# Kernel optimization log

Hardware: AMD Instinct MI355X
Metric: run time of the kernel (lower is better)

Reference implementation:

```python
import jax, jax.numpy as jnp
from jax import lax
import numpy as np

SCORE_THRESH = 0.05
NMS_THRESH = 0.5
MAX_DET = 100
MIN_SIZE = 0.01
BBOX_CLIP = float(np.log(1000.0 / 16.0))
NEG = -1e10


def setup_inputs() -> dict:
    key = jax.random.key(0)
    ks = jax.random.split(key, 12)
    N, IN, REP, C = 2000, 256 * 7 * 7, 1024, 91
    box_features = jax.random.normal(ks[0], (N, IN), jnp.float32)
    x1 = jax.random.uniform(ks[1], (N,), jnp.float32, 0.0, 1000.0)
    y1 = jax.random.uniform(ks[2], (N,), jnp.float32, 0.0, 600.0)
    bw = jax.random.uniform(ks[3], (N,), jnp.float32, 16.0, 200.0)
    bh = jax.random.uniform(ks[4], (N,), jnp.float32, 16.0, 180.0)
    proposals = jnp.stack([x1, y1, x1 + bw, y1 + bh], axis=1)
    W1 = jax.random.normal(ks[5], (IN, REP), jnp.float32) * 0.01
    b1 = jnp.zeros((REP,), jnp.float32)
    W2 = jax.random.normal(ks[6], (REP, REP), jnp.float32) * 0.03
    b2 = jnp.zeros((REP,), jnp.float32)
    Wc = jax.random.normal(ks[7], (REP, C), jnp.float32) * 0.1
    bc = jax.random.normal(ks[8], (C,), jnp.float32) * 0.5
    Wr = jax.random.normal(ks[9], (REP, 4 * C), jnp.float32) * 0.01
    br = jnp.zeros((4 * C,), jnp.float32)
    return dict(box_features=box_features, proposals=proposals,
                W1=W1, b1=b1, W2=W2, b2=b2, Wc=Wc, bc=bc, Wr=Wr, br=br,
                image_h=800, image_w=1216)


def _nms(boxes, scores):
    """Greedy NMS with fixed trip count; scores already masked to NEG for invalid."""
    M = boxes.shape[0]
    areas = (boxes[:, 2] - boxes[:, 0]) * (boxes[:, 3] - boxes[:, 1])
    idxs = jnp.arange(M)

    def step(sm, _):
        i = jnp.argmax(sm)
        valid = sm[i] > NEG * 0.5
        b = boxes[i]
        xx1 = jnp.maximum(b[0], boxes[:, 0]); yy1 = jnp.maximum(b[1], boxes[:, 1])
        xx2 = jnp.minimum(b[2], boxes[:, 2]); yy2 = jnp.minimum(b[3], boxes[:, 3])
        inter = jnp.clip(xx2 - xx1, 0.0) * jnp.clip(yy2 - yy1, 0.0)
        iou = inter / (areas[i] + areas - inter + 1e-9)
        suppress = (iou > NMS_THRESH) | (idxs == i)
        sm = jnp.where(valid, jnp.where(suppress, NEG, sm), sm)
        return sm, jnp.where(valid, i, -1)

    _, keep = lax.scan(step, scores, None, length=MAX_DET)
    return keep  # [MAX_DET] int, -1 for padding


def reference(box_features, proposals, W1, b1, W2, b2, Wc, bc, Wr, br, image_h, image_w):
    N = box_features.shape[0]
    C = Wc.shape[1]
    # box head MLP (Linear+ReLU x2) and predictors
    h = jax.nn.relu(box_features @ W1 + b1)
    h = jax.nn.relu(h @ W2 + b2)
    class_logits = h @ Wc + bc                      # [N, C]
    box_reg = (h @ Wr + br).reshape(N, C, 4)        # [N, C, 4]
    # box decode (weights 10,10,5,5) against proposals
    pw = proposals[:, 2] - proposals[:, 0]
    ph = proposals[:, 3] - proposals[:, 1]
    pcx = proposals[:, 0] + 0.5 * pw
    pcy = proposals[:, 1] + 0.5 * ph
    dx = box_reg[..., 0] / 10.0
    dy = box_reg[..., 1] / 10.0
    dw = jnp.minimum(box_reg[..., 2] / 5.0, BBOX_CLIP)
    dh = jnp.minimum(box_reg[..., 3] / 5.0, BBOX_CLIP)
    cx = dx * pw[:, None] + pcx[:, None]
    cy = dy * ph[:, None] + pcy[:, None]
    w = jnp.exp(dw) * pw[:, None]
    hh = jnp.exp(dh) * ph[:, None]
    boxes = jnp.stack([cx - 0.5 * w, cy - 0.5 * hh, cx + 0.5 * w, cy + 0.5 * hh], axis=-1)
    scores = jax.nn.softmax(class_logits, axis=-1)
    # clip to image
    Wim = jnp.float32(image_w); Him = jnp.float32(image_h)
    boxes = jnp.stack([jnp.clip(boxes[..., 0], 0.0, Wim),
                       jnp.clip(boxes[..., 1], 0.0, Him),
                       jnp.clip(boxes[..., 2], 0.0, Wim),
                       jnp.clip(boxes[..., 3], 0.0, Him)], axis=-1)
    # drop background class, flatten to [N*(C-1)]
    boxes = boxes[:, 1:].reshape(-1, 4)
    scores = scores[:, 1:].reshape(-1)
    labels = jnp.broadcast_to(jnp.arange(1, C, dtype=jnp.int32), (N, C - 1)).reshape(-1)
    # score threshold + remove small boxes (as masking, static shapes)
    bw = boxes[:, 2] - boxes[:, 0]
    bh = boxes[:, 3] - boxes[:, 1]
    valid = (scores > SCORE_THRESH) & (bw >= MIN_SIZE) & (bh >= MIN_SIZE)
    sm = jnp.where(valid, scores, NEG)
    # class-aware (batched) NMS via per-class coordinate offsets
    off = labels.astype(boxes.dtype) * (jnp.maximum(Wim, Him) + 1.0)
    keep = _nms(boxes + off[:, None], sm)
    mask = keep >= 0
    idx = jnp.maximum(keep, 0)
    out_boxes = jnp.take(boxes, idx, axis=0) * mask[:, None]
    out_scores = jnp.take(scores, idx) * mask
    out_labels = jnp.take(labels, idx) * mask.astype(jnp.int32)
    return out_boxes, out_scores, out_labels
```

## Files before the change

kernel.cpp:

```cpp
#include <hip/hip_runtime.h>

#define TM 128
#define TN 128
#define TKK 16
#define CPC 2000
#define SPC 100
#define NCLS 90

typedef __attribute__((ext_vector_type(8))) short bf16x8;
typedef __attribute__((ext_vector_type(4))) float f32x4;

__device__ __forceinline__ unsigned short f2bf_rne(float f) {
    unsigned u = __float_as_uint(f);
    return (unsigned short)((u + 0x7FFFu + ((u >> 16) & 1u)) >> 16);
}
__device__ __forceinline__ unsigned short f2bf_trunc(float f) {
    return (unsigned short)(__float_as_uint(f) >> 16);
}
__device__ __forceinline__ float bfhi_f32(float f) {
    return __uint_as_float(__float_as_uint(f) & 0xFFFF0000u);
}
__device__ __forceinline__ void async_load16(const void* g, void* l) {
    __builtin_amdgcn_global_load_lds((const __attribute__((address_space(1))) unsigned int*)g,
                                     (__attribute__((address_space(3))) unsigned int*)l, 16, 0, 0);
}

__global__ __launch_bounds__(256) void split_transpose(
    const float* __restrict__ W, unsigned short* __restrict__ Thi,
    unsigned short* __restrict__ Tlo, int K, int N)
{
    __shared__ float tile[32][33];
    const int kt = blockIdx.x * 32, nt = blockIdx.y * 32;
    const int tx = threadIdx.x & 31, ty = threadIdx.x >> 5;
#pragma unroll
    for (int j = 0; j < 4; ++j) {
        int k = kt + ty + j * 8, n = nt + tx;
        tile[ty + j * 8][tx] = (k < K && n < N) ? W[(size_t)k * N + n] : 0.f;
    }
    __syncthreads();
#pragma unroll
    for (int j = 0; j < 4; ++j) {
        int n = nt + ty + j * 8, k = kt + tx;
        if (n < N && k < K) {
            float f = tile[tx][ty + j * 8];
            Thi[(size_t)n * K + k] = f2bf_trunc(f);
            Tlo[(size_t)n * K + k] = f2bf_rne(f - bfhi_f32(f));
        }
    }
}

__global__ __launch_bounds__(256) void split_transpose2(
    const float* __restrict__ Wa, const float* __restrict__ Wb, int Na, int Nb,
    unsigned short* __restrict__ Thi, unsigned short* __restrict__ Tlo, int K)
{
    const int N = Na + Nb;
    __shared__ float tile[32][33];
    const int kt = blockIdx.x * 32, nt = blockIdx.y * 32;
    const int tx = threadIdx.x & 31, ty = threadIdx.x >> 5;
#pragma unroll
    for (int j = 0; j < 4; ++j) {
        int k = kt + ty + j * 8, n = nt + tx;
        float v = 0.f;
        if (k < K && n < N)
            v = (n < Na) ? Wa[(size_t)k * Na + n] : Wb[(size_t)k * Nb + (n - Na)];
        tile[ty + j * 8][tx] = v;
    }
    __syncthreads();
#pragma unroll
    for (int j = 0; j < 4; ++j) {
        int n = nt + ty + j * 8, k = kt + tx;
        if (n < N && k < K) {
            float f = tile[tx][ty + j * 8];
            Thi[(size_t)n * K + k] = f2bf_trunc(f);
            Tlo[(size_t)n * K + k] = f2bf_rne(f - bfhi_f32(f));
        }
    }
}

__global__ __launch_bounds__(256) void gemm_bf16x3(
    const float* __restrict__ A, const unsigned short* __restrict__ Bhi,
    const unsigned short* __restrict__ Blo, float* __restrict__ C,
    int M, int N, int K, int klen)
{
    __shared__ unsigned short Ah[4096], Al[4096], Bh[4096], Bl[4096];
    const int tid = threadIdx.x;
    const int wv = tid >> 6, ln = tid & 63;
    const int q = ln >> 4, lm = ln & 15;
    const int m0 = blockIdx.y * 128, n0 = blockIdx.x * 128;
    const int k0 = blockIdx.z * klen, k1 = k0 + klen;
    const int arow_t = (wv >> 1) * 64, bcol_t = (wv & 1) * 64;

    f32x4 acc[4][4];
#pragma unroll
    for (int i = 0; i < 4; ++i)
#pragma unroll
        for (int j = 0; j < 4; ++j) acc[i][j] = (f32x4)0.f;

    const int r = tid >> 1, h = tid & 1;
    const bool arow_ok = (m0 + r) < M;
    const float* Arow = A + (size_t)(m0 + r) * K + h * 16;

    for (int kt = k0; kt < k1; kt += 32) {
#pragma unroll
        for (int i = 0; i < 2; ++i) {
            int c = i * 256 + wv * 64 + ln;
            int kq = c >> 7;
            int gn = n0 + (c & 127); if (gn >= N) gn = N - 1;
            async_load16(Bhi + (size_t)gn * K + kt + kq * 8, &Bh[(size_t)(i * 256 + wv * 64) * 8]);
            async_load16(Blo + (size_t)gn * K + kt + kq * 8, &Bl[(size_t)(i * 256 + wv * 64) * 8]);
        }
        float f[16];
        if (arow_ok) {
            const float4* ap = reinterpret_cast<const float4*>(Arow + kt);
#pragma unroll
            for (int e = 0; e < 4; ++e) {
                float4 v = ap[e];
                f[e * 4 + 0] = v.x; f[e * 4 + 1] = v.y; f[e * 4 + 2] = v.z; f[e * 4 + 3] = v.w;
            }
        } else {
#pragma unroll
            for (int e = 0; e < 16; ++e) f[e] = 0.f;
        }
        bf16x8 h0, h1, l0, l1;
#pragma unroll
        for (int e = 0; e < 8; ++e) {
            h0[e] = (short)f2bf_trunc(f[e]);
            h1[e] = (short)f2bf_trunc(f[e + 8]);
            l0[e] = (short)f2bf_rne(f[e] - bfhi_f32(f[e]));
            l1[e] = (short)f2bf_rne(f[e + 8] - bfhi_f32(f[e + 8]));
        }
        *(bf16x8*)&Ah[(size_t)((h * 2 + 0) * 128 + r) * 8] = h0;
        *(bf16x8*)&Ah[(size_t)((h * 2 + 1) * 128 + r) * 8] = h1;
        *(bf16x8*)&Al[(size_t)((h * 2 + 0) * 128 + r) * 8] = l0;
        *(bf16x8*)&Al[(size_t)((h * 2 + 1) * 128 + r) * 8] = l1;
        __syncthreads();

        bf16x8 afh[4], afl[4], bfh[4], bfl[4];
#pragma unroll
        for (int mi = 0; mi < 4; ++mi) {
            int c = q * 128 + arow_t + mi * 16 + lm;
            afh[mi] = *(const bf16x8*)&Ah[(size_t)c * 8];
            afl[mi] = *(const bf16x8*)&Al[(size_t)c * 8];
        }
#pragma unroll
        for (int ni = 0; ni < 4; ++ni) {
            int c = q * 128 + bcol_t + ni * 16 + lm;
            bfh[ni] = *(const bf16x8*)&Bh[(size_t)c * 8];
            bfl[ni] = *(const bf16x8*)&Bl[(size_t)c * 8];
        }
#pragma unroll
        for (int mi = 0; mi < 4; ++mi)
#pragma unroll
            for (int ni = 0; ni < 4; ++ni) {
                acc[mi][ni] = __builtin_amdgcn_mfma_f32_16x16x32_bf16(afh[mi], bfh[ni], acc[mi][ni], 0, 0, 0);
                acc[mi][ni] = __builtin_amdgcn_mfma_f32_16x16x32_bf16(afl[mi], bfh[ni], acc[mi][ni], 0, 0, 0);
                acc[mi][ni] = __builtin_amdgcn_mfma_f32_16x16x32_bf16(afh[mi], bfl[ni], acc[mi][ni], 0, 0, 0);
            }
        __syncthreads();
    }

    float* Cz = C + (size_t)blockIdx.z * (size_t)M * (size_t)N;
#pragma unroll
    for (int mi = 0; mi < 4; ++mi)
#pragma unroll
        for (int ni = 0; ni < 4; ++ni)
#pragma unroll
            for (int ri = 0; ri < 4; ++ri) {
                int rr = m0 + arow_t + mi * 16 + q * 4 + ri;
                int cc = n0 + bcol_t + ni * 16 + lm;
                if (rr < M && cc < N) Cz[(size_t)rr * N + cc] = acc[mi][ni][ri];
            }
}

__global__ __launch_bounds__(256) void gemm_f32(
    const float* __restrict__ A, const float* __restrict__ B,
    const float* __restrict__ bias, float* __restrict__ C,
    int M, int N, int K, int ksplit, int relu)
{
    __shared__ float As[TKK][TM + 4];
    __shared__ float Bs[TKK][TN + 4];
    const int tid = threadIdx.x;
    const int tx = tid & 15, ty = tid >> 4;
    const int m0 = blockIdx.y * TM, n0 = blockIdx.x * TN;
    const int z = blockIdx.z;
    const int kstart = z * ksplit;
    const int kend = (kstart + ksplit < K) ? (kstart + ksplit) : K;
    float* Cz = C + (size_t)z * (size_t)M * (size_t)N;
    const bool nvec = ((N & 3) == 0);

    float acc[8][8];
#pragma unroll
    for (int i = 0; i < 8; ++i)
#pragma unroll
        for (int j = 0; j < 8; ++j) acc[i][j] = 0.f;

    for (int kt = kstart; kt < kend; kt += TKK) {
#pragma unroll
        for (int l = 0; l < 2; ++l) {
            int idx = tid + l * 256;
            int rr = idx >> 2, kq = idx & 3;
            float4 v = make_float4(0.f, 0.f, 0.f, 0.f);
            int gr = m0 + rr;
            if (gr < M)
                v = *reinterpret_cast<const float4*>(A + (size_t)gr * K + kt + (kq << 2));
            As[(kq << 2) + 0][rr] = v.x;
            As[(kq << 2) + 1][rr] = v.y;
            As[(kq << 2) + 2][rr] = v.z;
            As[(kq << 2) + 3][rr] = v.w;
        }
#pragma unroll
        for (int l = 0; l < 2; ++l) {
            int idx = tid + l * 256;
            int kk = idx >> 5, nq = idx & 31;
            int gn = n0 + (nq << 2);
            const float* bp = B + (size_t)(kt + kk) * N + gn;
            float4 v;
            if (nvec && gn + 3 < N) {
                v = *reinterpret_cast<const float4*>(bp);
            } else {
                v.x = (gn + 0 < N) ? bp[0] : 0.f;
                v.y = (gn + 1 < N) ? bp[1] : 0.f;
                v.z = (gn + 2 < N) ? bp[2] : 0.f;
                v.w = (gn + 3 < N) ? bp[3] : 0.f;
            }
            *reinterpret_cast<float4*>(&Bs[kk][nq << 2]) = v;
        }
        __syncthreads();
#pragma unroll
        for (int kk = 0; kk < TKK; ++kk) {
            float a[8], b[8];
            *reinterpret_cast<float4*>(&a[0]) = *reinterpret_cast<const float4*>(&As[kk][ty * 8]);
            *reinterpret_cast<float4*>(&a[4]) = *reinterpret_cast<const float4*>(&As[kk][ty * 8 + 4]);
            *reinterpret_cast<float4*>(&b[0]) = *reinterpret_cast<const float4*>(&Bs[kk][tx * 4]);
            *reinterpret_cast<float4*>(&b[4]) = *reinterpret_cast<const float4*>(&Bs[kk][64 + tx * 4]);
#pragma unroll
            for (int i = 0; i < 8; ++i)
#pragma unroll
                for (int j = 0; j < 8; ++j)
                    acc[i][j] = fmaf(a[i], b[j], acc[i][j]);
        }
        __syncthreads();
    }
#pragma unroll
    for (int i = 0; i < 8; ++i) {
        int gr = m0 + ty * 8 + i;
        if (gr >= M) continue;
#pragma unroll
        for (int j = 0; j < 8; ++j) {
            int gc = n0 + ((j < 4) ? (tx * 4 + j) : (64 + tx * 4 + (j - 4)));
            if (gc >= N) continue;
            float v = acc[i][j];
            if (bias) v += bias[gc];
            if (relu) v = fmaxf(v, 0.f);
            Cz[(size_t)gr * N + gc] = v;
        }
    }
}

__global__ void combine_bias_act(const float* __restrict__ P, const float* __restrict__ bias,
                                 float* __restrict__ H, int total, int N, int nsplit,
                                 int pstride, int relu)
{
    int i = blockIdx.x * blockDim.x + threadIdx.x;
    if (i >= total) return;
    float s = P[i];
    for (int j = 1; j < nsplit; ++j) s += P[i + (size_t)j * (size_t)pstride];
    s += bias[i % N];
    if (relu) s = fmaxf(s, 0.f);
    H[i] = s;
}

__global__ void combine_head(const float* __restrict__ P, const float* __restrict__ bc,
                             const float* __restrict__ br, float* __restrict__ H,
                             int total, int nsplit, int pstride)
{
    int i = blockIdx.x * blockDim.x + threadIdx.x;
    if (i >= total) return;
    float s = P[i];
    for (int j = 1; j < nsplit; ++j) s += P[i + (size_t)j * (size_t)pstride];
    int col = i % 455;
    s += (col < 91) ? bc[col] : br[col - 91];
    H[i] = s;
}

__device__ __forceinline__ float scalar_dim(const int* p)
{
    int iv = *p;
    return (iv > 0 && iv < (1 << 20)) ? (float)iv : *reinterpret_cast<const float*>(p);
}

__global__ __launch_bounds__(128) void decode_compact(
    const float* __restrict__ logits, int lstr, const float* __restrict__ breg, int bstr,
    const float4* __restrict__ proposals, const int* __restrict__ ihp,
    const int* __restrict__ iwp,
    float4* __restrict__ cbox, float* __restrict__ cscore, int* __restrict__ cn,
    int* __restrict__ ccnt)
{
    const int n = blockIdx.x;
    const int c = threadIdx.x;
    __shared__ float sl[91];
    __shared__ float s_max, s_sum;
    if (c < 91) sl[c] = logits[(size_t)n * lstr + c];
    __syncthreads();
    if (c == 0) {
        float m = sl[0];
        for (int i = 1; i < 91; ++i) m = fmaxf(m, sl[i]);
        float s = 0.f;
        for (int i = 0; i < 91; ++i) s += expf(sl[i] - m);
        s_max = m; s_sum = s;
    }
    __syncthreads();
    if (c < 1 || c >= 91) return;

    const float score = expf(sl[c] - s_max) / s_sum;
    const float Wim = scalar_dim(iwp), Him = scalar_dim(ihp);
    float4 p = proposals[n];
    float pw = p.z - p.x, ph = p.w - p.y;
    float pcx = p.x + 0.5f * pw, pcy = p.y + 0.5f * ph;
    const float* r4 = breg + (size_t)n * bstr + c * 4;
    float dxv = r4[0] / 10.f, dyv = r4[1] / 10.f;
    const float BCLIP = 4.135166556742356f;
    float dwv = fminf(r4[2] / 5.f, BCLIP);
    float dhv = fminf(r4[3] / 5.f, BCLIP);
    float cx = dxv * pw + pcx, cy = dyv * ph + pcy;
    float w = expf(dwv) * pw, hh = expf(dhv) * ph;
    float x1 = cx - 0.5f * w, y1 = cy - 0.5f * hh;
    float x2 = cx + 0.5f * w, y2 = cy + 0.5f * hh;
    x1 = fminf(fmaxf(x1, 0.f), Wim);
    y1 = fminf(fmaxf(y1, 0.f), Him);
    x2 = fminf(fmaxf(x2, 0.f), Wim);
    y2 = fminf(fmaxf(y2, 0.f), Him);
    float bw = x2 - x1, bh = y2 - y1;
    if (score > 0.05f && bw >= 0.01f && bh >= 0.01f) {
        int cls = c - 1;
        int pos = atomicAdd(&ccnt[cls], 1);
        if (pos < CPC) {
            cbox[cls * CPC + pos] = make_float4(x1, y1, x2, y2);
            cscore[cls * CPC + pos] = score;
            cn[cls * CPC + pos] = n;
        }
    }
}

__global__ __launch_bounds__(256) void nms_class(
    const float4* __restrict__ cbox, const float* __restrict__ cscore,
    const int* __restrict__ cn, const int* __restrict__ ccnt,
    float4* __restrict__ sbox, float* __restrict__ sscore,
    unsigned long long* __restrict__ skey, int* __restrict__ scnt)
{
    const int cls = blockIdx.x;
    const int tid = threadIdx.x;
    int cnt = ccnt[cls]; if (cnt > CPC) cnt = CPC;

    __shared__ float4 cb[CPC];
    __shared__ unsigned long long keys[CPC];
    __shared__ unsigned long long red[4];
    __shared__ float4 selsh;
    __shared__ int selidx_sh;

    for (int i = tid; i < cnt; i += 256) {
        cb[i] = cbox[cls * CPC + i];
        unsigned int sb = __float_as_uint(cscore[cls * CPC + i]);
        sb ^= (sb >> 31) ? 0xFFFFFFFFu : 0x80000000u;
        unsigned int flat = (unsigned)cn[cls * CPC + i] * 90u + (unsigned)cls;
        keys[i] = ((unsigned long long)sb << 32) | (unsigned long long)(0xFFFFFFFFu - flat);
    }
    __syncthreads();

    int sel = 0;
    while (sel < SPC) {
        unsigned long long best = 0ull;
        for (int i = tid; i < cnt; i += 256) {
            unsigned long long k = keys[i];
            if (k > best) best = k;
        }
#pragma unroll
        for (int d = 32; d >= 1; d >>= 1) {
            unsigned long long o = __shfl_down(best, d, 64);
            if (o > best) best = o;
        }
        if ((tid & 63) == 0) red[tid >> 6] = best;
        __syncthreads();
        unsigned long long gbest = red[0];
        if (red[1] > gbest) gbest = red[1];
        if (red[2] > gbest) gbest = red[2];
        if (red[3] > gbest) gbest = red[3];
        if (gbest == 0ull) break;
        for (int i = tid; i < cnt; i += 256)
            if (keys[i] == gbest) { selsh = cb[i]; selidx_sh = i; }
        __syncthreads();
        float4 s = selsh;
        const int si = selidx_sh;
        const float sa = (s.z - s.x) * (s.w - s.y);
        if (tid == 0) {
            sbox[cls * SPC + sel] = s;
            unsigned int sb = (unsigned int)(gbest >> 32);
            sb ^= (sb >> 31) ? 0x80000000u : 0xFFFFFFFFu;
            sscore[cls * SPC + sel] = __uint_as_float(sb);
            skey[cls * SPC + sel] = gbest;
        }
        for (int i = tid; i < cnt; i += 256) {
            float4 b = cb[i];
            float xx1 = fmaxf(s.x, b.x), yy1 = fmaxf(s.y, b.y);
            float xx2 = fminf(s.z, b.z), yy2 = fminf(s.w, b.w);
            float inter = fmaxf(xx2 - xx1, 0.f) * fmaxf(yy2 - yy1, 0.f);
            float area = (b.z - b.x) * (b.w - b.y);
            if (3.f * inter > sa + area + 1e-9f || i == si) keys[i] = 0ull;
        }
        ++sel;
        __syncthreads();
    }
    if (tid == 0) scnt[cls] = sel;
}

__global__ __launch_bounds__(128) void nms_merge(
    const float4* __restrict__ sbox, const float* __restrict__ sscore,
    const unsigned long long* __restrict__ skey, const int* __restrict__ scnt,
    float* __restrict__ out)
{
    const int tid = threadIdx.x;
    __shared__ int head[NCLS];
    __shared__ unsigned long long red[2];
    __shared__ int selc_sh;
    if (tid < NCLS) head[tid] = 0;
    __syncthreads();

    for (int k = 0; k < 100; ++k) {
        unsigned long long key = 0ull;
        if (tid < NCLS && head[tid] < scnt[tid]) key = skey[tid * SPC + head[tid]];
        unsigned long long mykey = key;
#pragma unroll
        for (int d = 32; d >= 1; d >>= 1) {
            unsigned long long o = __shfl_down(key, d, 64);
            if (o > key) key = o;
        }
        if ((tid & 63) == 0) red[tid >> 6] = key;
        if (tid == 0) selc_sh = -1;
        __syncthreads();
        unsigned long long gbest = red[0] > red[1] ? red[0] : red[1];
        if (gbest != 0ull && mykey == gbest) selc_sh = tid;
        __syncthreads();
        const int c = selc_sh;
        if (tid == 0) {
            if (c >= 0) {
                int h = head[c];
                float4 b = sbox[c * SPC + h];
                out[k * 4 + 0] = b.x; out[k * 4 + 1] = b.y;
                out[k * 4 + 2] = b.z; out[k * 4 + 3] = b.w;
                out[400 + k] = sscore[c * SPC + h];
                out[500 + k] = (float)(c + 1);
            } else {
                out[k * 4 + 0] = 0.f; out[k * 4 + 1] = 0.f;
                out[k * 4 + 2] = 0.f; out[k * 4 + 3] = 0.f;
                out[400 + k] = 0.f; out[500 + k] = 0.f;
            }
        }
        if (c >= 0 && tid == c) head[c]++;
        __syncthreads();
    }
}

extern "C" void kernel_launch(void* const* d_in, const int* in_sizes, int n_in,
                              void* d_out, int out_size, void* d_ws, size_t ws_size,
                              hipStream_t stream)
{
    const float* bf    = (const float*)d_in[0];
    const float* props = (const float*)d_in[1];
    const float* W1    = (const float*)d_in[2];
    const float* b1    = (const float*)d_in[3];
    const float* W2    = (const float*)d_in[4];
    const float* b2    = (const float*)d_in[5];
    const float* Wc    = (const float*)d_in[6];
    const float* bc    = (const float*)d_in[7];
    const float* Wr    = (const float*)d_in[8];
    const float* br    = (const float*)d_in[9];
    const int*   ihp   = (const int*)d_in[10];
    const int*   iwp   = (const int*)d_in[11];
    float* ws  = (float*)d_ws;
    float* out = (float*)d_out;

    const size_t MN   = 2000ull * 1024ull;
    const size_t NLOG = 2000ull * 91ull;
    const size_t NREG = 2000ull * 364ull;
    const size_t NHEAD = 2000ull * 455ull;
    const size_t ws_floats = ws_size / 4;

    const size_t BT1F = 1024ull * 12544ull / 2;
    const size_t WT2F = 1024ull * 1024ull / 2;
    const size_t WHF  = 455ull * 1024ull / 2;
    const size_t NMSF = (size_t)NCLS * CPC * 6 + (size_t)NCLS * SPC * 7 + 256;
    const size_t PF   = 4 * MN;
    const size_t NEED = 2 * BT1F + 2 * WT2F + 2 * WHF + 2 * MN + NHEAD + NMSF + PF + 64;

    if (ws_floats >= NEED) {
        unsigned short* BT1hi = (unsigned short*)ws;
        unsigned short* BT1lo = (unsigned short*)(ws + BT1F);
        unsigned short* WT2hi = (unsigned short*)(ws + 2 * BT1F);
        unsigned short* WT2lo = (unsigned short*)(ws + 2 * BT1F + WT2F);
        unsigned short* WHhi  = (unsigned short*)(ws + 2 * BT1F + 2 * WT2F);
        unsigned short* WHlo  = (unsigned short*)(ws + 2 * BT1F + 2 * WT2F + WHF);
        float* H1   = ws + 2 * BT1F + 2 * WT2F + 2 * WHF;
        float* H2   = H1 + MN;
        float* HEAD = H2 + MN;
        float* CBOX   = HEAD + NHEAD;
        float* CSCORE = CBOX + (size_t)NCLS * CPC * 4;
        int*   CN     = (int*)(CSCORE + (size_t)NCLS * CPC);
        float* SBOX   = (float*)(CN + (size_t)NCLS * CPC);
        float* SSCORE = SBOX + (size_t)NCLS * SPC * 4;
        unsigned long long* SKEY = (unsigned long long*)(SSCORE + (size_t)NCLS * SPC);
        int*   CCNT = (int*)(SKEY + (size_t)NCLS * SPC);
        int*   SCNT = CCNT + NCLS;
        float* P = (float*)(SCNT + NCLS + 62);

        split_transpose<<<dim3(392, 32), 256, 0, stream>>>(W1, BT1hi, BT1lo, 12544, 1024);
        split_transpose<<<dim3(32, 32), 256, 0, stream>>>(W2, WT2hi, WT2lo, 1024, 1024);
        split_transpose2<<<dim3(32, 15), 256, 0, stream>>>(Wc, Wr, 91, 364, WHhi, WHlo, 1024);
        gemm_bf16x3<<<dim3(8, 16, 4), 256, 0, stream>>>(bf, BT1hi, BT1lo, P,
                                                        2000, 1024, 12544, 3136);
        combine_bias_act<<<(int)((MN + 255) / 256), 256, 0, stream>>>(P, b1, H1,
                                                        (int)MN, 1024, 4, (int)MN, 1);
        gemm_bf16x3<<<dim3(8, 16, 4), 256, 0, stream>>>(H1, WT2hi, WT2lo, P,
                                                        2000, 1024, 1024, 256);
        combine_bias_act<<<(int)((MN + 255) / 256), 256, 0, stream>>>(P, b2, H2,
                                                        (int)MN, 1024, 4, (int)MN, 1);
        gemm_bf16x3<<<dim3(4, 16, 8), 256, 0, stream>>>(H2, WHhi, WHlo, P,
                                                        2000, 455, 1024, 128);
        combine_head<<<(int)((NHEAD + 255) / 256), 256, 0, stream>>>(P, bc, br, HEAD,
                                                        (int)NHEAD, 8, (int)NHEAD);
        hipMemsetAsync(CCNT, 0, 2 * NCLS * sizeof(int), stream);
        decode_compact<<<2000, 128, 0, stream>>>(HEAD, 455, HEAD + 91, 455,
                                                 (const float4*)props, ihp, iwp,
                                                 (float4*)CBOX, CSCORE, CN, CCNT);
        nms_class<<<NCLS, 256, 0, stream>>>((const float4*)CBOX, CSCORE, CN, CCNT,
                                            (float4*)SBOX, SSCORE, SKEY, SCNT);
        nms_merge<<<1, 128, 0, stream>>>((const float4*)SBOX, SSCORE, SKEY, SCNT, out);
        return;
    }

    const size_t NMSF2 = (size_t)NCLS * CPC * 6 + (size_t)NCLS * SPC * 7 + 256;
    const size_t TAILF = 2 * MN + NLOG + NREG + NMSF2;
    int z1 = 2;
    if (ws_floats >= TAILF + 8 * MN) z1 = 8;
    else if (ws_floats >= TAILF + 4 * MN) z1 = 4;
    const size_t REUSE = (size_t)z1 * MN;
    int zh = (REUSE >= 8 * NREG) ? 8 : 4;

    float* P      = ws;
    float* H1     = P + REUSE;
    float* H2     = H1 + MN;
    float* LOG    = H2 + MN;
    float* BREG   = LOG + NLOG;
    float* CBOX   = BREG + NREG;
    float* CSCORE = CBOX + (size_t)NCLS * CPC * 4;
    int*   CN     = (int*)(CSCORE + (size_t)NCLS * CPC);
    float* SBOX   = (float*)(CN + (size_t)NCLS * CPC);
    float* SSCORE = SBOX + (size_t)NCLS * SPC * 4;
    unsigned long long* SKEY = (unsigned long long*)(SSCORE + (size_t)NCLS * SPC);
    int*   CCNT   = (int*)(SKEY + (size_t)NCLS * SPC);
    int*   SCNT   = CCNT + NCLS;

    gemm_f32<<<dim3(8, 16, z1), 256, 0, stream>>>(bf, W1, nullptr, P,
                                                  2000, 1024, 12544, 12544 / z1, 0);
    combine_bias_act<<<(int)((MN + 255) / 256), 256, 0, stream>>>(P, b1, H1,
                                                  (int)MN, 1024, z1, (int)MN, 1);
    gemm_f32<<<dim3(8, 16, 4), 256, 0, stream>>>(H1, W2, nullptr, P,
                                                 2000, 1024, 1024, 256, 0);
    combine_bias_act<<<(int)((MN + 255) / 256), 256, 0, stream>>>(P, b2, H2,
                                                 (int)MN, 1024, 4, (int)MN, 1);
    gemm_f32<<<dim3(1, 16, zh), 256, 0, stream>>>(H2, Wc, nullptr, P,
                                                  2000, 91, 1024, 1024 / zh, 0);
    combine_bias_act<<<(int)((NLOG + 255) / 256), 256, 0, stream>>>(P, bc, LOG,
                                                  (int)NLOG, 91, zh, (int)NLOG, 0);
    gemm_f32<<<dim3(3, 16, zh), 256, 0, stream>>>(H2, Wr, nullptr, P,
                                                  2000, 364, 1024, 1024 / zh, 0);
    combine_bias_act<<<(int)((NREG + 255) / 256), 256, 0, stream>>>(P, br, BREG,
                                                  (int)NREG, 364, zh, (int)NREG, 0);
    hipMemsetAsync(CCNT, 0, 2 * NCLS * sizeof(int), stream);
    decode_compact<<<2000, 128, 0, stream>>>(LOG, 91, BREG, 364,
                                             (const float4*)props, ihp, iwp,
                                             (float4*)CBOX, CSCORE, CN, CCNT);
    nms_class<<<NCLS, 256, 0, stream>>>((const float4*)CBOX, CSCORE, CN, CCNT,
                                        (float4*)SBOX, SSCORE, SKEY, SCNT);
    nms_merge<<<1, 128, 0, stream>>>((const float4*)SBOX, SSCORE, SKEY, SCNT, out);
}
```

Baseline: 761.6 us.

## Shrink GEMM tiles to 64x128, swizzle LDS, pre-split activations into bf16 hi/lo

The bf16x3 GEMMs now use 64x128 block tiles (each wave computes 64x32), doubling the block count and setting occupancy hints with launch_bounds(256,4). LDS layouts use an XOR swizzle to reduce bank conflicts. For the second and third GEMMs, the combine kernel writes the activations already split into bf16 hi/lo, so the GEMM loads A asynchronously into LDS and skips the per-tile conversion. The trade-off is more global reloads of B from the smaller M tiles and more, smaller blocks.

Result: no change. 751.0 us (-1.4%).

```diff
diff --git a/kernel.cpp b/kernel.cpp
--- a/kernel.cpp
+++ b/kernel.cpp
@@ -1,11 +1,11 @@
 #include <hip/hip_runtime.h>
 
+#define CPC 2000
+#define SPC 100
+#define NCLS 90
 #define TM 128
 #define TN 128
 #define TKK 16
-#define CPC 2000
-#define SPC 100
-#define NCLS 90
 
 typedef __attribute__((ext_vector_type(8))) short bf16x8;
 typedef __attribute__((ext_vector_type(4))) float f32x4;
@@ -24,6 +24,7 @@
     __builtin_amdgcn_global_load_lds((const __attribute__((address_space(1))) unsigned int*)g,
                                      (__attribute__((address_space(3))) unsigned int*)l, 16, 0, 0);
 }
+__device__ __forceinline__ int swz(int c) { return c ^ ((c >> 3) & 3); }
 
 __global__ __launch_bounds__(256) void split_transpose(
     const float* __restrict__ W, unsigned short* __restrict__ Thi,
@@ -77,81 +78,75 @@
     }
 }
 
-__global__ __launch_bounds__(256) void gemm_bf16x3(
+__global__ __launch_bounds__(256, 4) void gemm_bf16x3_f32a(
     const float* __restrict__ A, const unsigned short* __restrict__ Bhi,
     const unsigned short* __restrict__ Blo, float* __restrict__ C,
     int M, int N, int K, int klen)
 {
-    __shared__ unsigned short Ah[4096], Al[4096], Bh[4096], Bl[4096];
+    __shared__ unsigned short Ah[2048], Al[2048], Bh[4096], Bl[4096];
     const int tid = threadIdx.x;
     const int wv = tid >> 6, ln = tid & 63;
     const int q = ln >> 4, lm = ln & 15;
-    const int m0 = blockIdx.y * 128, n0 = blockIdx.x * 128;
+    const int m0 = blockIdx.y * 64, n0 = blockIdx.x * 128;
     const int k0 = blockIdx.z * klen, k1 = k0 + klen;
-    const int arow_t = (wv >> 1) * 64, bcol_t = (wv & 1) * 64;
-
-    f32x4 acc[4][4];
+    const int bcol_t = wv * 32;
+
+    f32x4 acc[4][2];
 #pragma unroll
     for (int i = 0; i < 4; ++i)
 #pragma unroll
-        for (int j = 0; j < 4; ++j) acc[i][j] = (f32x4)0.f;
-
-    const int r = tid >> 1, h = tid & 1;
-    const bool arow_ok = (m0 + r) < M;
-    const float* Arow = A + (size_t)(m0 + r) * K + h * 16;
+        for (int j = 0; j < 2; ++j) acc[i][j] = (f32x4)0.f;
+
+    const int r = tid >> 2, h = tid & 3;
+    int gr = m0 + r; if (gr >= M) gr = M - 1;
+    const float* Arow = A + (size_t)gr * K + h * 8;
+    const int apc = swz(tid);
+
+    unsigned bsrc[2];
+#pragma unroll
+    for (int i = 0; i < 2; ++i) {
+        int s = i * 256 + tid;
+        int gn = n0 + (s >> 2); if (gn >= N) gn = N - 1;
+        int qe = (s & 3) ^ ((s >> 3) & 3);
+        bsrc[i] = (unsigned)gn * (unsigned)K + (unsigned)(qe * 8);
+    }
 
     for (int kt = k0; kt < k1; kt += 32) {
 #pragma unroll
         for (int i = 0; i < 2; ++i) {
-            int c = i * 256 + wv * 64 + ln;
-            int kq = c >> 7;
-            int gn = n0 + (c & 127); if (gn >= N) gn = N - 1;
-            async_load16(Bhi + (size_t)gn * K + kt + kq * 8, &Bh[(size_t)(i * 256 + wv * 64) * 8]);
-            async_load16(Blo + (size_t)gn * K + kt + kq * 8, &Bl[(size_t)(i * 256 + wv * 64) * 8]);
-        }
-        float f[16];
-        if (arow_ok) {
-            const float4* ap = reinterpret_cast<const float4*>(Arow + kt);
-#pragma unroll
-            for (int e = 0; e < 4; ++e) {
-                float4 v = ap[e];
-                f[e * 4 + 0] = v.x; f[e * 4 + 1] = v.y; f[e * 4 + 2] = v.z; f[e * 4 + 3] = v.w;
-            }
-        } else {
-#pragma unroll
-            for (int e = 0; e < 16; ++e) f[e] = 0.f;
-        }
-        bf16x8 h0, h1, l0, l1;
+            async_load16(Bhi + bsrc[i] + kt, &Bh[(i * 256 + wv * 64) * 8]);
+            async_load16(Blo + bsrc[i] + kt, &Bl[(i * 256 + wv * 64) * 8]);
+        }
+        float4 v0 = *reinterpret_cast<const float4*>(Arow + kt);
+        float4 v1 = *reinterpret_cast<const float4*>(Arow + kt + 4);
+        float f[8] = {v0.x, v0.y, v0.z, v0.w, v1.x, v1.y, v1.z, v1.w};
+        bf16x8 hi, lo;
 #pragma unroll
         for (int e = 0; e < 8; ++e) {
-            h0[e] = (short)f2bf_trunc(f[e]);
-            h1[e] = (short)f2bf_trunc(f[e + 8]);
-            l0[e] = (short)f2bf_rne(f[e] - bfhi_f32(f[e]));
-            l1[e] = (short)f2bf_rne(f[e + 8] - bfhi_f32(f[e + 8]));
-        }
-        *(bf16x8*)&Ah[(size_t)((h * 2 + 0) * 128 + r) * 8] = h0;
-        *(bf16x8*)&Ah[(size_t)((h * 2 + 1) * 128 + r) * 8] = h1;
-        *(bf16x8*)&Al[(size_t)((h * 2 + 0) * 128 + r) * 8] = l0;
-        *(bf16x8*)&Al[(size_t)((h * 2 + 1) * 128 + r) * 8] = l1;
-        __syncthreads();
-
-        bf16x8 afh[4], afl[4], bfh[4], bfl[4];
+            hi[e] = (short)f2bf_trunc(f[e]);
+            lo[e] = (short)f2bf_rne(f[e] - bfhi_f32(f[e]));
+        }
+        *(bf16x8*)&Ah[apc * 8] = hi;
+        *(bf16x8*)&Al[apc * 8] = lo;
+        __syncthreads();
+
+        bf16x8 afh[4], afl[4], bfh[2], bfl[2];
 #pragma unroll
         for (int mi = 0; mi < 4; ++mi) {
-            int c = q * 128 + arow_t + mi * 16 + lm;
-            afh[mi] = *(const bf16x8*)&Ah[(size_t)c * 8];
-            afl[mi] = *(const bf16x8*)&Al[(size_t)c * 8];
-        }
-#pragma unroll
-        for (int ni = 0; ni < 4; ++ni) {
-            int c = q * 128 + bcol_t + ni * 16 + lm;
-            bfh[ni] = *(const bf16x8*)&Bh[(size_t)c * 8];
-            bfl[ni] = *(const bf16x8*)&Bl[(size_t)c * 8];
+            int p = swz((mi * 16 + lm) * 4 + q);
+            afh[mi] = *(const bf16x8*)&Ah[p * 8];
+            afl[mi] = *(const bf16x8*)&Al[p * 8];
+        }
+#pragma unroll
+        for (int ni = 0; ni < 2; ++ni) {
+            int p = swz((bcol_t + ni * 16 + lm) * 4 + q);
+            bfh[ni] = *(const bf16x8*)&Bh[p * 8];
+            bfl[ni] = *(const bf16x8*)&Bl[p * 8];
         }
 #pragma unroll
         for (int mi = 0; mi < 4; ++mi)
 #pragma unroll
-            for (int ni = 0; ni < 4; ++ni) {
+            for (int ni = 0; ni < 2; ++ni) {
                 acc[mi][ni] = __builtin_amdgcn_mfma_f32_16x16x32_bf16(afh[mi], bfh[ni], acc[mi][ni], 0, 0, 0);
                 acc[mi][ni] = __builtin_amdgcn_mfma_f32_16x16x32_bf16(afl[mi], bfh[ni], acc[mi][ni], 0, 0, 0);
                 acc[mi][ni] = __builtin_amdgcn_mfma_f32_16x16x32_bf16(afh[mi], bfl[ni], acc[mi][ni], 0, 0, 0);
@@ -163,10 +158,91 @@
 #pragma unroll
     for (int mi = 0; mi < 4; ++mi)
 #pragma unroll
-        for (int ni = 0; ni < 4; ++ni)
+        for (int ni = 0; ni < 2; ++ni)
 #pragma unroll
             for (int ri = 0; ri < 4; ++ri) {
-                int rr = m0 + arow_t + mi * 16 + q * 4 + ri;
+                int rr = m0 + mi * 16 + q * 4 + ri;
+                int cc = n0 + bcol_t + ni * 16 + lm;
+                if (rr < M && cc < N) Cz[(size_t)rr * N + cc] = acc[mi][ni][ri];
+            }
+}
+
+__global__ __launch_bounds__(256, 4) void gemm_bf16x3_sa(
+    const unsigned short* __restrict__ Ahi_g, const unsigned short* __restrict__ Alo_g,
+    const unsigned short* __restrict__ Bhi, const unsigned short* __restrict__ Blo,
+    float* __restrict__ C, int M, int N, int K, int klen)
+{
+    __shared__ unsigned short Ah[2048], Al[2048], Bh[4096], Bl[4096];
+    const int tid = threadIdx.x;
+    const int wv = tid >> 6, ln = tid & 63;
+    const int q = ln >> 4, lm = ln & 15;
+    const int m0 = blockIdx.y * 64, n0 = blockIdx.x * 128;
+    const int k0 = blockIdx.z * klen, k1 = k0 + klen;
+    const int bcol_t = wv * 32;
+
+    f32x4 acc[4][2];
+#pragma unroll
+    for (int i = 0; i < 4; ++i)
+#pragma unroll
+        for (int j = 0; j < 2; ++j) acc[i][j] = (f32x4)0.f;
+
+    {
+    }
+    int agr = m0 + (tid >> 2); if (agr >= M) agr = M - 1;
+    const int aqe = (tid & 3) ^ ((tid >> 3) & 3);
+    const unsigned asrc = (unsigned)agr * (unsigned)K + (unsigned)(aqe * 8);
+
+    unsigned bsrc[2];
+#pragma unroll
+    for (int i = 0; i < 2; ++i) {
+        int s = i * 256 + tid;
+        int gn = n0 + (s >> 2); if (gn >= N) gn = N - 1;
+        int qe = (s & 3) ^ ((s >> 3) & 3);
+        bsrc[i] = (unsigned)gn * (unsigned)K + (unsigned)(qe * 8);
+    }
+
+    for (int kt = k0; kt < k1; kt += 32) {
+        async_load16(Ahi_g + asrc + kt, &Ah[(wv * 64) * 8]);
+        async_load16(Alo_g + asrc + kt, &Al[(wv * 64) * 8]);
+#pragma unroll
+        for (int i = 0; i < 2; ++i) {
+            async_load16(Bhi + bsrc[i] + kt, &Bh[(i * 256 + wv * 64) * 8]);
+            async_load16(Blo + bsrc[i] + kt, &Bl[(i * 256 + wv * 64) * 8]);
+        }
+        __syncthreads();
+
+        bf16x8 afh[4], afl[4], bfh[2], bfl[2];
+#pragma unroll
+        for (int mi = 0; mi < 4; ++mi) {
+            int p = swz((mi * 16 + lm) * 4 + q);
+            afh[mi] = *(const bf16x8*)&Ah[p * 8];
+            afl[mi] = *(const bf16x8*)&Al[p * 8];
+        }
+#pragma unroll
+        for (int ni = 0; ni < 2; ++ni) {
+            int p = swz((bcol_t + ni * 16 + lm) * 4 + q);
+            bfh[ni] = *(const bf16x8*)&Bh[p * 8];
+            bfl[ni] = *(const bf16x8*)&Bl[p * 8];
+        }
+#pragma unroll
+        for (int mi = 0; mi < 4; ++mi)
+#pragma unroll
+            for (int ni = 0; ni < 2; ++ni) {
+                acc[mi][ni] = __builtin_amdgcn_mfma_f32_16x16x32_bf16(afh[mi], bfh[ni], acc[mi][ni], 0, 0, 0);
+                acc[mi][ni] = __builtin_amdgcn_mfma_f32_16x16x32_bf16(afl[mi], bfh[ni], acc[mi][ni], 0, 0, 0);
+                acc[mi][ni] = __builtin_amdgcn_mfma_f32_16x16x32_bf16(afh[mi], bfl[ni], acc[mi][ni], 0, 0, 0);
+            }
+        __syncthreads();
+    }
+
+    float* Cz = C + (size_t)blockIdx.z * (size_t)M * (size_t)N;
+#pragma unroll
+    for (int mi = 0; mi < 4; ++mi)
+#pragma unroll
+        for (int ni = 0; ni < 2; ++ni)
+#pragma unroll
+            for (int ri = 0; ri < 4; ++ri) {
+                int rr = m0 + mi * 16 + q * 4 + ri;
                 int cc = n0 + bcol_t + ni * 16 + lm;
                 if (rr < M && cc < N) Cz[(size_t)rr * N + cc] = acc[mi][ni][ri];
             }
@@ -200,9 +276,9 @@
             int idx = tid + l * 256;
             int rr = idx >> 2, kq = idx & 3;
             float4 v = make_float4(0.f, 0.f, 0.f, 0.f);
-            int gr = m0 + rr;
-            if (gr < M)
-                v = *reinterpret_cast<const float4*>(A + (size_t)gr * K + kt + (kq << 2));
+            int grr = m0 + rr;
+            if (grr < M)
+                v = *reinterpret_cast<const float4*>(A + (size_t)grr * K + kt + (kq << 2));
             As[(kq << 2) + 0][rr] = v.x;
             As[(kq << 2) + 1][rr] = v.y;
             As[(kq << 2) + 2][rr] = v.z;
@@ -243,8 +319,8 @@
     }
 #pragma unroll
     for (int i = 0; i < 8; ++i) {
-        int gr = m0 + ty * 8 + i;
-        if (gr >= M) continue;
+        int grr = m0 + ty * 8 + i;
+        if (grr >= M) continue;
 #pragma unroll
         for (int j = 0; j < 8; ++j) {
             int gc = n0 + ((j < 4) ? (tx * 4 + j) : (64 + tx * 4 + (j - 4)));
@@ -252,7 +328,7 @@
             float v = acc[i][j];
             if (bias) v += bias[gc];
             if (relu) v = fmaxf(v, 0.f);
-            Cz[(size_t)gr * N + gc] = v;
+            Cz[(size_t)grr * N + gc] = v;
         }
     }
 }
@@ -268,6 +344,20 @@
     s += bias[i % N];
     if (relu) s = fmaxf(s, 0.f);
     H[i] = s;
+}
+
+__global__ void combine_bias_split(const float* __restrict__ P, const float* __restrict__ bias,
+                                   unsigned short* __restrict__ Hhi, unsigned short* __restrict__ Hlo,
+                                   int total, int N, int nsplit, int pstride, int relu)
+{
+    int i = blockIdx.x * blockDim.x + threadIdx.x;
+    if (i >= total) return;
+    float s = P[i];
+    for (int j = 1; j < nsplit; ++j) s += P[i + (size_t)j * (size_t)pstride];
+    s += bias[i % N];
+    if (relu) s = fmaxf(s, 0.f);
+    Hhi[i] = f2bf_trunc(s);
+    Hlo[i] = f2bf_rne(s - bfhi_f32(s));
 }
 
 __global__ void combine_head(const float* __restrict__ P, const float* __restrict__ bc,
@@ -512,21 +602,26 @@
         int*   SCNT = CCNT + NCLS;
         float* P = (float*)(SCNT + NCLS + 62);
 
+        unsigned short* H1hi = (unsigned short*)H1;
+        unsigned short* H1lo = H1hi + MN;
+        unsigned short* H2hi = (unsigned short*)H2;
+        unsigned short* H2lo = H2hi + MN;
+
         split_transpose<<<dim3(392, 32), 256, 0, stream>>>(W1, BT1hi, BT1lo, 12544, 1024);
         split_transpose<<<dim3(32, 32), 256, 0, stream>>>(W2, WT2hi, WT2lo, 1024, 1024);
         split_transpose2<<<dim3(32, 15), 256, 0, stream>>>(Wc, Wr, 91, 364, WHhi, WHlo, 1024);
-        gemm_bf16x3<<<dim3(8, 16, 4), 256, 0, stream>>>(bf, BT1hi, BT1lo, P,
-                                                        2000, 1024, 12544, 3136);
-        combine_bias_act<<<(int)((MN + 255) / 256), 256, 0, stream>>>(P, b1, H1,
-                                                        (int)MN, 1024, 4, (int)MN, 1);
-        gemm_bf16x3<<<dim3(8, 16, 4), 256, 0, stream>>>(H1, WT2hi, WT2lo, P,
-                                                        2000, 1024, 1024, 256);
-        combine_bias_act<<<(int)((MN + 255) / 256), 256, 0, stream>>>(P, b2, H2,
-                                                        (int)MN, 1024, 4, (int)MN, 1);
-        gemm_bf16x3<<<dim3(4, 16, 8), 256, 0, stream>>>(H2, WHhi, WHlo, P,
-                                                        2000, 455, 1024, 128);
+        gemm_bf16x3_f32a<<<dim3(8, 32, 4), 256, 0, stream>>>(bf, BT1hi, BT1lo, P,
+                                                             2000, 1024, 12544, 3136);
+        combine_bias_split<<<(int)((MN + 255) / 256), 256, 0, stream>>>(P, b1, H1hi, H1lo,
+                                                             (int)MN, 1024, 4, (int)MN, 1);
+        gemm_bf16x3_sa<<<dim3(8, 32, 4), 256, 0, stream>>>(H1hi, H1lo, WT2hi, WT2lo, P,
+                                                           2000, 1024, 1024, 256);
+        combine_bias_split<<<(int)((MN + 255) / 256), 256, 0, stream>>>(P, b2, H2hi, H2lo,
+                                                             (int)MN, 1024, 4, (int)MN, 1);
+        gemm_bf16x3_sa<<<dim3(4, 32, 8), 256, 0, stream>>>(H2hi, H2lo, WHhi, WHlo, P,
+                                                           2000, 455, 1024, 128);
         combine_head<<<(int)((NHEAD + 255) / 256), 256, 0, stream>>>(P, bc, br, HEAD,
-                                                        (int)NHEAD, 8, (int)NHEAD);
+                                                             (int)NHEAD, 8, (int)NHEAD);
         hipMemsetAsync(CCNT, 0, 2 * NCLS * sizeof(int), stream);
         decode_compact<<<2000, 128, 0, stream>>>(HEAD, 455, HEAD + 91, 455,
                                                  (const float4*)props, ihp, iwp,
```
